# Kernel tuning notes

Measured on AMD Instinct MI355X. Metric: run time of the kernel, lower is better.

Reference implementation:

```python
import jax, jax.numpy as jnp
import numpy as np

N_NODES = 100000
N_EDGES = 3200000


def _spmm(edge_row, edge_col, edge_val, h):
    # out[i] = sum_{e: row[e]==i} val[e] * h[col[e]]
    msgs = edge_val[:, None] * h[edge_col]  # [E, F]
    return jax.ops.segment_sum(msgs, edge_row, num_segments=N_NODES)


def _gc_layer(x, W, b, edge_row, edge_col, edge_val):
    # GraphConvolution: support = x @ W; out = spmm(adj, support) + b
    support = x @ W
    return _spmm(edge_row, edge_col, edge_val, support) + b


def setup_inputs() -> dict:
    key = jax.random.key(0)
    ks = jax.random.split(key, 8)
    F_IN, HID, C = 512, 256, 40
    x = jax.random.normal(ks[0], (N_NODES, F_IN), dtype=jnp.float32)
    W1 = jax.random.normal(ks[1], (F_IN, HID), dtype=jnp.float32) * (1.0 / np.sqrt(F_IN))
    b1 = jnp.zeros((HID,), dtype=jnp.float32)
    W2 = jax.random.normal(ks[2], (HID, C), dtype=jnp.float32) * (1.0 / np.sqrt(HID))
    b2 = jnp.zeros((C,), dtype=jnp.float32)
    edge_row = jax.random.randint(ks[3], (N_EDGES,), 0, N_NODES, dtype=jnp.int32)
    edge_col = jax.random.randint(ks[4], (N_EDGES,), 0, N_NODES, dtype=jnp.int32)
    edge_val = jax.random.uniform(ks[5], (N_EDGES,), dtype=jnp.float32) * 0.05
    return {"x": x, "W1": W1, "b1": b1, "W2": W2, "b2": b2,
            "edge_row": edge_row, "edge_col": edge_col, "edge_val": edge_val}


def reference(x, W1, b1, W2, b2, edge_row, edge_col, edge_val):
    h = jax.nn.relu(_gc_layer(x, W1, b1, edge_row, edge_col, edge_val))
    # dropout: inference mode (training=False) -> identity
    logits = _gc_layer(h, W2, b2, edge_row, edge_col, edge_val)
    return (jax.nn.log_softmax(logits, axis=1), jax.nn.softmax(logits, axis=1))
```

## Files before the change

kernel.cpp:

```cpp
#include <hip/hip_runtime.h>
#include <hip/hip_bf16.h>

#define N_NODES 100000
#define N_EDGES 3200000
#define F_IN    512
#define HID     256
#define C_OUT   40

#define RPB     512
#define BSHIFT  9
#define NBUCK   196
#define CAP     20480
#define GSTR    16

typedef unsigned short u16;
typedef unsigned char  u8;
typedef unsigned int   u32;
typedef __attribute__((ext_vector_type(8))) short bf16x8;
typedef __attribute__((ext_vector_type(4))) float f32x4;
typedef __attribute__((ext_vector_type(2))) float f32x2;

__device__ __forceinline__ u16 f2bf(float f) {
    u32 x = __float_as_uint(f);
    return (u16)((x + 0x7fffu + ((x >> 16) & 1u)) >> 16);
}
__device__ __forceinline__ u32 pk2(float lo, float hi) {
    return (u32)f2bf(lo) | ((u32)f2bf(hi) << 16);
}


__global__ __launch_bounds__(256) void k_prep(const float* __restrict__ W1,
                                              const float* __restrict__ W2,
                                              u16* __restrict__ W1t,
                                              u16* __restrict__ W2t,
                                              int* __restrict__ gfill) {
    int b = blockIdx.x, t = threadIdx.x;
    if (b < 512) {
        int i = b * 256 + t;
        int k = i >> 8, n = i & 255;
        W1t[(size_t)n * F_IN + k] = f2bf(W1[i]);
    } else if (b < 576) {
        int i = (b - 512) * 256 + t;
        int n = i >> 8, k = i & 255;
        W2t[i] = (n < C_OUT) ? f2bf(W2[k * C_OUT + n]) : (u16)0;
    } else {
        for (int j = t; j < NBUCK * GSTR; j += 256) gfill[j] = 0;
    }
}


__global__ __launch_bounds__(1024) void k_p1(const int* __restrict__ row,
                                             const int* __restrict__ col,
                                             const float* __restrict__ val,
                                             int* __restrict__ gfill,
                                             int2* __restrict__ bpack) {
    __shared__ int hist[NBUCK];
    __shared__ int base[NBUCK];
    int t = threadIdx.x;
    for (int j = t; j < NBUCK; j += 1024) hist[j] = 0;
    __syncthreads();
    int e0 = blockIdx.x * 4096;
    int bin[4], key[4], lr[4];
    float vl[4];
#pragma unroll
    for (int u = 0; u < 4; u++) {
        int i = e0 + u * 1024 + t;
        if (i < N_EDGES) {
            int r = row[i];
            bin[u] = r >> BSHIFT;
            key[u] = (col[i] << BSHIFT) | (r & (RPB - 1));
            vl[u] = val[i];
            lr[u] = atomicAdd(&hist[bin[u]], 1);
        } else {
            bin[u] = -1;
        }
    }
    __syncthreads();
    for (int j = t; j < NBUCK; j += 1024)
        base[j] = atomicAdd(&gfill[j * GSTR], hist[j]);
    __syncthreads();
#pragma unroll
    for (int u = 0; u < 4; u++) {
        if (bin[u] >= 0) {
            int p = base[bin[u]] + lr[u];
            if (p < CAP)
                bpack[(size_t)bin[u] * CAP + p] = make_int2(key[u], __float_as_int(vl[u]));
        }
    }
}

__global__ __launch_bounds__(1024) void k_p2(const int2* __restrict__ bpack,
                                             const int* __restrict__ gfill,
                                             int2* __restrict__ cpack,
                                             int* __restrict__ row_off) {
    __shared__ int bb[256];
    __shared__ int cnt[RPB];
    __shared__ int sc[RPB];
    __shared__ int rbase[RPB];
    int b = blockIdx.x, t = threadIdx.x;
    if (t < 256) bb[t] = (t < NBUCK) ? gfill[t * GSTR] : 0;
    __syncthreads();
    for (int off = 1; off < 256; off <<= 1) {
        int x = 0;
        if (t < 256 && t >= off) x = bb[t - off];
        __syncthreads();
        if (t < 256) bb[t] += x;
        __syncthreads();
    }
    int gbase = (b == 0) ? 0 : bb[b - 1];
    if (b == NBUCK - 1 && t == 0) row_off[N_NODES] = bb[NBUCK - 1];
    int n = gfill[b * GSTR];
    if (n > CAP) n = CAP;
    if (t < RPB) cnt[t] = 0;
    __syncthreads();
    int key[20], lr[20];
    float v[20];
#pragma unroll
    for (int u = 0; u < 20; u++) {
        int i = u * 1024 + t;
        if (i < n) {
            int2 p = bpack[(size_t)b * CAP + i];
            key[u] = p.x;
            v[u] = __int_as_float(p.y);
            lr[u] = atomicAdd(&cnt[key[u] & (RPB - 1)], 1);
        } else {
            key[u] = -1;
        }
    }
    __syncthreads();
    if (t < RPB) sc[t] = cnt[t];
    __syncthreads();
    for (int off = 1; off < RPB; off <<= 1) {
        int x = 0;
        if (t < RPB && t >= off) x = sc[t - off];
        __syncthreads();
        if (t < RPB) sc[t] += x;
        __syncthreads();
    }
    if (t < RPB) rbase[t] = (t == 0) ? 0 : sc[t - 1];
    __syncthreads();
    int g0 = b * RPB;
    if (t < RPB && (g0 + t) < N_NODES) row_off[g0 + t] = gbase + rbase[t];
#pragma unroll
    for (int u = 0; u < 20; u++) {
        if (key[u] >= 0) {
            int pos = gbase + rbase[key[u] & (RPB - 1)] + lr[u];
            cpack[pos] = make_int2(key[u] >> BSHIFT, __float_as_int(v[u]));
        }
    }
}


#define ASTR 40
#define BSTR 40

__global__ __launch_bounds__(512) void k_gemm1(const float* __restrict__ A,
                                               const u16* __restrict__ Bt,
                                               u8* __restrict__ Cf8, int M) {
    __shared__ u16 As[128 * ASTR];
    __shared__ u16 Bs[256 * BSTR];
    int tid = threadIdx.x;
    int bm = blockIdx.x * 128;
    int lane = tid & 63, wid = tid >> 6;
    int wm = wid >> 2, wn = wid & 3;

    int s_ar = tid >> 2;
    int s_ak = (tid & 3) * 8;
    int s_bn = tid >> 1;
    int s_bk = (tid & 1) * 16;

    bool arow_ok = (bm + s_ar) < M;
    const float* aptr = A + (size_t)(bm + s_ar) * F_IN + s_ak;
    const u16*   bptr = Bt + (size_t)s_bn * F_IN + s_bk;

    f32x4 acc[4][4];
#pragma unroll
    for (int i = 0; i < 4; i++)
#pragma unroll
        for (int j = 0; j < 4; j++) acc[i][j] = (f32x4){0.f, 0.f, 0.f, 0.f};

    int kg = lane >> 4;
    int r16 = lane & 15;

#pragma unroll 1
    for (int kt = 0; kt < F_IN / 32; kt++) {
        float4 ra0, ra1;
        int4 rb0, rb1;
        const float* ap = aptr + kt * 32;
        if (arow_ok) {
            ra0 = *(const float4*)ap;
            ra1 = *(const float4*)(ap + 4);
        } else {
            ra0 = make_float4(0.f, 0.f, 0.f, 0.f);
            ra1 = ra0;
        }
        const u16* bp = bptr + kt * 32;
        rb0 = *(const int4*)bp;
        rb1 = *(const int4*)(bp + 8);
        __syncthreads();
        int4 w;
        w.x = pk2(ra0.x, ra0.y);
        w.y = pk2(ra0.z, ra0.w);
        w.z = pk2(ra1.x, ra1.y);
        w.w = pk2(ra1.z, ra1.w);
        *(int4*)&As[s_ar * ASTR + s_ak] = w;
        *(int4*)&Bs[s_bn * BSTR + s_bk] = rb0;
        *(int4*)&Bs[s_bn * BSTR + s_bk + 8] = rb1;
        __syncthreads();
        bf16x8 a[4], b[4];
#pragma unroll
        for (int mt = 0; mt < 4; mt++)
            a[mt] = *(const bf16x8*)&As[(wm * 64 + mt * 16 + r16) * ASTR + kg * 8];
#pragma unroll
        for (int nt = 0; nt < 4; nt++)
            b[nt] = *(const bf16x8*)&Bs[(wn * 64 + nt * 16 + r16) * BSTR + kg * 8];
#pragma unroll
        for (int mt = 0; mt < 4; mt++)
#pragma unroll
            for (int nt = 0; nt < 4; nt++)
                acc[mt][nt] = __builtin_amdgcn_mfma_f32_16x16x32_bf16(
                    b[nt], a[mt], acc[mt][nt], 0, 0, 0);
    }

#pragma unroll
    for (int mt = 0; mt < 4; mt++) {
        int xr = bm + wm * 64 + mt * 16 + (lane & 15);
        if (xr < M) {
#pragma unroll
            for (int nt = 0; nt < 4; nt++) {
                int wc0 = wn * 64 + nt * 16 + (lane >> 4) * 4;
                u32 d = __builtin_amdgcn_cvt_pk_fp8_f32(acc[mt][nt][0], acc[mt][nt][1], 0u, false);
                d = __builtin_amdgcn_cvt_pk_fp8_f32(acc[mt][nt][2], acc[mt][nt][3], d, true);
                *(u32*)&Cf8[(size_t)xr * HID + wc0] = d;
            }
        }
    }
}


__global__ __launch_bounds__(256) void k_spmm1(const u8* __restrict__ Sf8,
                                               const int2* __restrict__ cpack,
                                               const int* __restrict__ row_off,
                                               const float* __restrict__ b1,
                                               u8* __restrict__ Hb8) {
    int lane = threadIdx.x & 63;
    int row = blockIdx.x * 4 + (threadIdx.x >> 6);
    int beg = __builtin_amdgcn_readfirstlane(row_off[row]);
    int end = __builtin_amdgcn_readfirstlane(row_off[row + 1]);
    int f4 = lane * 4;
    const u8* base = Sf8 + f4;
    float acc[4] = {};
    int e = beg;
    for (; e + 8 <= end; e += 8) {
        int2 q[8];
#pragma unroll
        for (int t = 0; t < 8; t++) q[t] = cpack[e + t];
#pragma unroll
        for (int t = 0; t < 8; t++) {
            float vv = __int_as_float(q[t].y);
            u32 w = *(const u32*)(base + (size_t)q[t].x * HID);
            f32x2 lo = __builtin_amdgcn_cvt_pk_f32_fp8(w, false);
            f32x2 hi = __builtin_amdgcn_cvt_pk_f32_fp8(w, true);
            acc[0] += vv * lo.x;
            acc[1] += vv * lo.y;
            acc[2] += vv * hi.x;
            acc[3] += vv * hi.y;
        }
    }
    for (; e < end; e++) {
        int2 q = cpack[e];
        float vv = __int_as_float(q.y);
        u32 w = *(const u32*)(base + (size_t)q.x * HID);
        f32x2 lo = __builtin_amdgcn_cvt_pk_f32_fp8(w, false);
        f32x2 hi = __builtin_amdgcn_cvt_pk_f32_fp8(w, true);
        acc[0] += vv * lo.x;
        acc[1] += vv * lo.y;
        acc[2] += vv * hi.x;
        acc[3] += vv * hi.y;
    }
    float4 b = *(const float4*)&b1[f4];
    float h0 = fmaxf(acc[0] + b.x, 0.f);
    float h1 = fmaxf(acc[1] + b.y, 0.f);
    float h2 = fmaxf(acc[2] + b.z, 0.f);
    float h3 = fmaxf(acc[3] + b.w, 0.f);
    u32 d = __builtin_amdgcn_cvt_pk_fp8_f32(h0, h1, 0u, false);
    d = __builtin_amdgcn_cvt_pk_fp8_f32(h2, h3, d, true);
    *(u32*)&Hb8[(size_t)row * HID + f4] = d;
}


#define G2STR 264

__global__ __launch_bounds__(256) void k_gemm2(const u8* __restrict__ Hb8,
                                               const u16* __restrict__ W2t,
                                               u8* __restrict__ S2f8) {
    __shared__ u16 As[64 * G2STR];
    int tid = threadIdx.x;
    int base = blockIdx.x * 64;
    {
        int r = tid >> 2, c0 = (tid & 3) * 64;
        const u8* src = Hb8 + (size_t)(base + r) * HID + c0;
        bool ok = (base + r) < N_NODES;
#pragma unroll
        for (int q = 0; q < 4; q++) {
            uint4 dv = ok ? *(const uint4*)(src + q * 16) : make_uint4(0, 0, 0, 0);
            u32 wbuf[8];
            u32 dd[4] = {dv.x, dv.y, dv.z, dv.w};
#pragma unroll
            for (int j = 0; j < 4; j++) {
                f32x2 lo = __builtin_amdgcn_cvt_pk_f32_fp8(dd[j], false);
                f32x2 hi = __builtin_amdgcn_cvt_pk_f32_fp8(dd[j], true);
                wbuf[2 * j]     = pk2(lo.x, lo.y);
                wbuf[2 * j + 1] = pk2(hi.x, hi.y);
            }
            *(int4*)&As[r * G2STR + c0 + q * 16]     = *(int4*)&wbuf[0];
            *(int4*)&As[r * G2STR + c0 + q * 16 + 8] = *(int4*)&wbuf[4];
        }
    }
    __syncthreads();
    int lane = tid & 63, wv = tid >> 6;
    int r16 = lane & 15, kg = lane >> 4;
    f32x4 acc[4];
#pragma unroll
    for (int nt = 0; nt < 4; nt++) acc[nt] = (f32x4){0.f, 0.f, 0.f, 0.f};
#pragma unroll
    for (int ks = 0; ks < 8; ks++) {
        bf16x8 a = *(const bf16x8*)&As[(wv * 16 + r16) * G2STR + ks * 32 + kg * 8];
#pragma unroll
        for (int nt = 0; nt < 4; nt++) {
            bf16x8 b = *(const bf16x8*)&W2t[(size_t)(nt * 16 + r16) * 256 + ks * 32 + kg * 8];
            acc[nt] = __builtin_amdgcn_mfma_f32_16x16x32_bf16(b, a, acc[nt], 0, 0, 0);
        }
    }
    int hr = base + wv * 16 + (lane & 15);
    if (hr < N_NODES) {
#pragma unroll
        for (int nt = 0; nt < 3; nt++) {
            int cls0 = nt * 16 + (lane >> 4) * 4;
            if (cls0 < C_OUT) {
                u32 d = __builtin_amdgcn_cvt_pk_fp8_f32(acc[nt][0], acc[nt][1], 0u, false);
                d = __builtin_amdgcn_cvt_pk_fp8_f32(acc[nt][2], acc[nt][3], d, true);
                *(u32*)&S2f8[(size_t)hr * C_OUT + cls0] = d;
            }
        }
    }
}


__global__ __launch_bounds__(256) void k_spmm2(const u8* __restrict__ S2f8,
                                               const int2* __restrict__ cpack,
                                               const int* __restrict__ row_off,
                                               const float* __restrict__ b2,
                                               float* __restrict__ out_ls,
                                               float* __restrict__ out_sm) {
    __shared__ float red[4][64][4];
    int tid = threadIdx.x;
    int lane = tid & 63, wv = tid >> 6;
    int row = blockIdx.x * 4 + wv;
    int beg = __builtin_amdgcn_readfirstlane(row_off[row]);
    int end = __builtin_amdgcn_readfirstlane(row_off[row + 1]);
    int g = lane / 10;
    int cb = (lane % 10) * 4;
    bool act = lane < 60;
    float acc[4] = {};
    for (int e0 = beg; e0 < end; e0 += 6) {
        int ei = e0 + g;
        bool ok = act && (ei < end);
        int2 q = cpack[ok ? ei : beg];
        float vv = ok ? __int_as_float(q.y) : 0.f;
        u32 w = *(const u32*)(S2f8 + (size_t)q.x * C_OUT + cb);
        f32x2 lo = __builtin_amdgcn_cvt_pk_f32_fp8(w, false);
        f32x2 hi = __builtin_amdgcn_cvt_pk_f32_fp8(w, true);
        acc[0] += vv * lo.x;
        acc[1] += vv * lo.y;
        acc[2] += vv * hi.x;
        acc[3] += vv * hi.y;
    }
#pragma unroll
    for (int j = 0; j < 4; j++) red[wv][lane][j] = acc[j];
    __builtin_amdgcn_s_waitcnt(0);
    float v;
    if (lane < C_OUT) {
        int sl = lane >> 2, j = lane & 3;
        float s = 0.f;
#pragma unroll
        for (int gg = 0; gg < 6; gg++) s += red[wv][gg * 10 + sl][j];
        v = s + b2[lane];
    } else {
        v = -1e30f;
    }
    float mx = v;
    for (int s = 32; s; s >>= 1) mx = fmaxf(mx, __shfl_xor(mx, s));
    float e2 = (lane < C_OUT) ? __expf(v - mx) : 0.f;
    float sum = e2;
    for (int s = 32; s; s >>= 1) sum += __shfl_xor(sum, s);
    float ls = v - mx - __logf(sum);
    float sm = e2 / sum;
    if (lane < C_OUT) {
        out_ls[(size_t)row * C_OUT + lane] = ls;
        out_sm[(size_t)row * C_OUT + lane] = sm;
    }
}


extern "C" void kernel_launch(void* const* d_in, const int* in_sizes, int n_in,
                              void* d_out, int out_size, void* d_ws, size_t ws_size,
                              hipStream_t stream) {
    const float* x    = (const float*)d_in[0];
    const float* W1   = (const float*)d_in[1];
    const float* b1   = (const float*)d_in[2];
    const float* W2   = (const float*)d_in[3];
    const float* b2   = (const float*)d_in[4];
    const int*   erow = (const int*)d_in[5];
    const int*   ecol = (const int*)d_in[6];
    const float* eval = (const float*)d_in[7];
    float* out = (float*)d_out;

    char* w = (char*)d_ws;
    auto alloc = [&](size_t bytes) {
        char* p = w;
        w += (bytes + 255) & ~(size_t)255;
        return p;
    };
    u8*    support = (u8*)   alloc((size_t)N_NODES * HID);
    u8*    hbuf8   = (u8*)   alloc((size_t)N_NODES * HID);
    int2*  cpack   = (int2*) alloc((size_t)N_EDGES * sizeof(int2));
    int2*  bpack   = (int2*) alloc((size_t)NBUCK * CAP * sizeof(int2));
    int*   row_off = (int*)  alloc((size_t)(N_NODES + 1) * sizeof(int));
    int*   gfill   = (int*)  alloc((size_t)NBUCK * GSTR * sizeof(int));
    u8*    S2f8    = (u8*)   alloc((size_t)N_NODES * C_OUT);
    u16*   W2t     = (u16*)  alloc((size_t)64 * 256 * sizeof(u16));
    u16*   W1t     = (u16*)  alloc((size_t)F_IN * HID * sizeof(u16));

    k_prep<<<577, 256, 0, stream>>>(W1, W2, W1t, W2t, gfill);

    int NB1 = (N_EDGES + 4095) / 4096;
    k_p1<<<NB1, 1024, 0, stream>>>(erow, ecol, eval, gfill, bpack);
    k_p2<<<NBUCK, 1024, 0, stream>>>(bpack, gfill, cpack, row_off);

    k_gemm1<<<(N_NODES + 127) / 128, 512, 0, stream>>>(x, W1t, support, N_NODES);
    k_spmm1<<<N_NODES / 4, 256, 0, stream>>>(support, cpack, row_off, b1, hbuf8);
    k_gemm2<<<(N_NODES + 63) / 64, 256, 0, stream>>>(hbuf8, W2t, S2f8);
    k_spmm2<<<N_NODES / 4, 256, 0, stream>>>(S2f8, cpack, row_off, b2,
                                             out, out + (size_t)N_NODES * C_OUT);
}
```

Before: 363.0 us.

## Store GEMM1 output in 32-feature slices and split SpMM1 across slices

GEMM1 now writes its fp8 output as eight column slices of 32 bytes per node instead of 256-byte rows. SpMM1 launches eight blocks per row group, one per slice. Within a wavefront, eight lanes cover a 32-byte slice and eight edges are processed in parallel, with a shuffle reduction at the end. The aim is a smaller gathered footprint per slice, for better cache locality, and more edge-level parallelism. The cost is reading the edge list eight times and extra shuffle work.

```diff
diff --git a/kernel.cpp b/kernel.cpp
--- a/kernel.cpp
+++ b/kernel.cpp
@@ -12,6 +12,7 @@
 #define NBUCK   196
 #define CAP     20480
 #define GSTR    16
+#define SLICE_B 32
 
 typedef unsigned short u16;
 typedef unsigned char  u8;
@@ -231,46 +232,37 @@
                 int wc0 = wn * 64 + nt * 16 + (lane >> 4) * 4;
                 u32 d = __builtin_amdgcn_cvt_pk_fp8_f32(acc[mt][nt][0], acc[mt][nt][1], 0u, false);
                 d = __builtin_amdgcn_cvt_pk_fp8_f32(acc[mt][nt][2], acc[mt][nt][3], d, true);
-                *(u32*)&Cf8[(size_t)xr * HID + wc0] = d;
+                *(u32*)&Cf8[(size_t)(wc0 >> 5) * ((size_t)N_NODES * SLICE_B)
+                            + (size_t)xr * SLICE_B + (wc0 & 31)] = d;
             }
         }
     }
 }
 
 
-__global__ __launch_bounds__(256) void k_spmm1(const u8* __restrict__ Sf8,
+__global__ __launch_bounds__(256) void k_spmm1(const u8* __restrict__ Sslc,
                                                const int2* __restrict__ cpack,
                                                const int* __restrict__ row_off,
                                                const float* __restrict__ b1,
                                                u8* __restrict__ Hb8) {
+    int bid = blockIdx.x;
+    int slice = bid & 7;
+    int rg = bid >> 3;
     int lane = threadIdx.x & 63;
-    int row = blockIdx.x * 4 + (threadIdx.x >> 6);
+    int row = rg * 4 + (threadIdx.x >> 6);
     int beg = __builtin_amdgcn_readfirstlane(row_off[row]);
     int end = __builtin_amdgcn_readfirstlane(row_off[row + 1]);
-    int f4 = lane * 4;
-    const u8* base = Sf8 + f4;
+    int g = lane >> 3;
+    int f = (lane & 7) * 4;
+    const u8* base = Sslc + (size_t)slice * ((size_t)N_NODES * SLICE_B) + f;
     float acc[4] = {};
-    int e = beg;
-    for (; e + 8 <= end; e += 8) {
-        int2 q[8];
-#pragma unroll
-        for (int t = 0; t < 8; t++) q[t] = cpack[e + t];
-#pragma unroll
-        for (int t = 0; t < 8; t++) {
-            float vv = __int_as_float(q[t].y);
-            u32 w = *(const u32*)(base + (size_t)q[t].x * HID);
-            f32x2 lo = __builtin_amdgcn_cvt_pk_f32_fp8(w, false);
-            f32x2 hi = __builtin_amdgcn_cvt_pk_f32_fp8(w, true);
-            acc[0] += vv * lo.x;
-            acc[1] += vv * lo.y;
-            acc[2] += vv * hi.x;
-            acc[3] += vv * hi.y;
-        }
-    }
-    for (; e < end; e++) {
-        int2 q = cpack[e];
-        float vv = __int_as_float(q.y);
-        u32 w = *(const u32*)(base + (size_t)q.x * HID);
+#pragma unroll 2
+    for (int e = beg; e < end; e += 8) {
+        int ei = e + g;
+        bool ok = ei < end;
+        int2 q = cpack[ok ? ei : beg];
+        float vv = ok ? __int_as_float(q.y) : 0.f;
+        u32 w = *(const u32*)(base + (size_t)q.x * SLICE_B);
         f32x2 lo = __builtin_amdgcn_cvt_pk_f32_fp8(w, false);
         f32x2 hi = __builtin_amdgcn_cvt_pk_f32_fp8(w, true);
         acc[0] += vv * lo.x;
@@ -278,14 +270,23 @@
         acc[2] += vv * hi.x;
         acc[3] += vv * hi.y;
     }
-    float4 b = *(const float4*)&b1[f4];
-    float h0 = fmaxf(acc[0] + b.x, 0.f);
-    float h1 = fmaxf(acc[1] + b.y, 0.f);
-    float h2 = fmaxf(acc[2] + b.z, 0.f);
-    float h3 = fmaxf(acc[3] + b.w, 0.f);
-    u32 d = __builtin_amdgcn_cvt_pk_fp8_f32(h0, h1, 0u, false);
-    d = __builtin_amdgcn_cvt_pk_fp8_f32(h2, h3, d, true);
-    *(u32*)&Hb8[(size_t)row * HID + f4] = d;
+#pragma unroll
+    for (int j = 0; j < 4; j++) {
+        acc[j] += __shfl_xor(acc[j], 8);
+        acc[j] += __shfl_xor(acc[j], 16);
+        acc[j] += __shfl_xor(acc[j], 32);
+    }
+    if (lane < 8) {
+        int fo = slice * SLICE_B + f;
+        float4 b = *(const float4*)&b1[fo];
+        float h0 = fmaxf(acc[0] + b.x, 0.f);
+        float h1 = fmaxf(acc[1] + b.y, 0.f);
+        float h2 = fmaxf(acc[2] + b.z, 0.f);
+        float h3 = fmaxf(acc[3] + b.w, 0.f);
+        u32 d = __builtin_amdgcn_cvt_pk_fp8_f32(h0, h1, 0u, false);
+        d = __builtin_amdgcn_cvt_pk_fp8_f32(h2, h3, d, true);
+        *(u32*)&Hb8[(size_t)row * HID + fo] = d;
+    }
 }
 
 
@@ -439,7 +440,7 @@
     k_p2<<<NBUCK, 1024, 0, stream>>>(bpack, gfill, cpack, row_off);
 
     k_gemm1<<<(N_NODES + 127) / 128, 512, 0, stream>>>(x, W1t, support, N_NODES);
-    k_spmm1<<<N_NODES / 4, 256, 0, stream>>>(support, cpack, row_off, b1, hbuf8);
+    k_spmm1<<<(N_NODES / 4) * 8, 256, 0, stream>>>(support, cpack, row_off, b1, hbuf8);
     k_gemm2<<<(N_NODES + 63) / 64, 256, 0, stream>>>(hbuf8, W2t, S2f8);
     k_spmm2<<<N_NODES / 4, 256, 0, stream>>>(S2f8, cpack, row_off, b2,
                                              out, out + (size_t)N_NODES * C_OUT);
```

Result: slower. 587.5 us (+61.9%).
